# Optimization experiments

Measured on AMD Instinct MI355X. Metric: run time of the kernel, lower is better.

## Reference

```python
import jax, jax.numpy as jnp
import numpy as np

B, C = 4096, 50257

def setup_inputs() -> dict:
    key = jax.random.key(0)
    k1, k2 = jax.random.split(key)
    pred = jax.random.normal(k1, (B, C), dtype=jnp.float32)
    target = jax.random.randint(k2, (B,), 0, C, dtype=jnp.int64)
    return {"pred": pred, "target": target}

def reference(pred, target):
    # log_softmax over classes, gather the target log-prob per sample,
    # then -1/B * sum (the original's per-class dict grouping sums to the same total).
    logp = jax.nn.log_softmax(pred, axis=1)          # [B, C]
    gathered = jnp.take_along_axis(logp, target[:, None], axis=1)[:, 0]  # [B]
    Bf = pred.shape[0]
    return -jnp.sum(gathered) / Bf
```

## Files before the change

kernel.cpp:

```cpp
#include <hip/hip_runtime.h>

#define NROWS 4096
#define NCLASS 50257
#define BLK 256
#define U 8
#define DEFER_THR 8.0f

__global__ __launch_bounds__(BLK) void ce_row_kernel(
    const float* __restrict__ pred,
    const int* __restrict__ target,
    float* __restrict__ row_loss) {
    const int row = blockIdx.x;
    const float* __restrict__ p = pred + (size_t)row * NCLASS;
    const int tid = threadIdx.x;

    float m = -3.4e38f;
    float l = 0.0f;

    const int head = (int)(((16u - (unsigned)((size_t)p & 15u)) & 15u) >> 2);
    if (tid < head) {
        m = p[tid];
        l = 1.0f;
    }

    const float4* __restrict__ pv = (const float4*)(p + head);
    const int nvec = (NCLASS - head) >> 2;

    const int CHUNK = U * BLK;
    const int nchunk = nvec / CHUNK;

    for (int c = 0; c < nchunk; ++c) {
        const int base = c * CHUNK + tid;

        float4 v[U];
        #pragma unroll
        for (int k = 0; k < U; ++k) v[k] = pv[base + k * BLK];

        float cm = -3.4e38f;
        #pragma unroll
        for (int k = 0; k < U; ++k) {
            cm = fmaxf(cm,
                       fmaxf(fmaxf(v[k].x, v[k].y), fmaxf(v[k].z, v[k].w)));
        }

        if (cm > m + DEFER_THR) {
            l *= __expf(m - cm);
            m = cm;
        }

        float s = 0.0f;
        #pragma unroll
        for (int k = 0; k < U; ++k) {
            s += __expf(v[k].x - m) + __expf(v[k].y - m)
               + __expf(v[k].z - m) + __expf(v[k].w - m);
        }
        l += s;
    }

    for (int i = nchunk * CHUNK + tid; i < nvec; i += BLK) {
        float4 v = pv[i];
        float vm = fmaxf(fmaxf(v.x, v.y), fmaxf(v.z, v.w));
        if (vm > m + DEFER_THR) {
            l *= __expf(m - vm);
            m = vm;
        }
        l += __expf(v.x - m) + __expf(v.y - m)
           + __expf(v.z - m) + __expf(v.w - m);
    }
    for (int j = head + (nvec << 2) + tid; j < NCLASS; j += BLK) {
        float x = p[j];
        if (x > m + DEFER_THR) {
            l *= __expf(m - x);
            m = x;
        }
        l += __expf(x - m);
    }

    #pragma unroll
    for (int off = 32; off > 0; off >>= 1) {
        float om = __shfl_down(m, off, 64);
        float ol = __shfl_down(l, off, 64);
        float nm = fmaxf(m, om);
        l = l * __expf(m - nm) + ol * __expf(om - nm);
        m = nm;
    }

    __shared__ float sm[BLK / 64];
    __shared__ float sl[BLK / 64];
    const int wave = tid >> 6;
    const int lane = tid & 63;
    if (lane == 0) { sm[wave] = m; sl[wave] = l; }
    __syncthreads();

    if (tid == 0) {
        m = sm[0]; l = sl[0];
        #pragma unroll
        for (int w = 1; w < BLK / 64; ++w) {
            float om = sm[w], ol = sl[w];
            float nm = fmaxf(m, om);
            l = l * __expf(m - nm) + ol * __expf(om - nm);
            m = nm;
        }
        const int t = target[row];
        row_loss[row] = -(p[t] - m - __logf(l));
    }
}

__global__ __launch_bounds__(BLK) void ce_reduce_kernel(
    const float* __restrict__ row_loss,
    float* __restrict__ out) {
    const int tid = threadIdx.x;
    float s = 0.0f;
    for (int i = tid; i < NROWS; i += BLK) s += row_loss[i];

    #pragma unroll
    for (int off = 32; off > 0; off >>= 1) s += __shfl_down(s, off, 64);

    __shared__ float sw[BLK / 64];
    if ((tid & 63) == 0) sw[tid >> 6] = s;
    __syncthreads();

    if (tid == 0) {
        float t = 0.0f;
        #pragma unroll
        for (int w = 0; w < BLK / 64; ++w) t += sw[w];
        out[0] = t * (1.0f / (float)NROWS);
    }
}

extern "C" void kernel_launch(void* const* d_in, const int* in_sizes, int n_in,
                              void* d_out, int out_size, void* d_ws, size_t ws_size,
                              hipStream_t stream) {
    const float* pred = (const float*)d_in[0];
    const int* target = (const int*)d_in[1];
    float* out = (float*)d_out;
    float* row_loss = (float*)d_ws;

    ce_row_kernel<<<NROWS, BLK, 0, stream>>>(pred, target, row_loss);
    ce_reduce_kernel<<<1, BLK, 0, stream>>>(row_loss, out);
}
```

Baseline: 1.014 ms.

## Split each row across four blocks and merge partial softmax stats in finisher

Each row's class range is split into four parts, each handled by its own block that writes a partial max and sum-exp to workspace. A single-block finish kernel merges the four partials per row, gathers the target logit and reduces to the loss. The unroll factor drops to 4 and launch bounds request 6 blocks per CU. This raises block count and occupancy to better saturate HBM bandwidth on the 823 MB read, at the cost of extra workspace traffic, unaligned head handling per part, and a heavier serial finisher that does 4096 scattered target gathers in one block.

```diff
diff --git a/kernel.cpp b/kernel.cpp
--- a/kernel.cpp
+++ b/kernel.cpp
@@ -3,15 +3,21 @@
 #define NROWS 4096
 #define NCLASS 50257
 #define BLK 256
-#define U 8
+#define NSPLIT 4
+#define QLEN ((NCLASS + NSPLIT - 1) / NSPLIT)
+#define U 4
 #define DEFER_THR 8.0f
 
-__global__ __launch_bounds__(BLK) void ce_row_kernel(
+__global__ __launch_bounds__(BLK, 6) void ce_part_kernel(
     const float* __restrict__ pred,
-    const int* __restrict__ target,
-    float* __restrict__ row_loss) {
-    const int row = blockIdx.x;
-    const float* __restrict__ p = pred + (size_t)row * NCLASS;
+    float* __restrict__ mbuf,
+    float* __restrict__ lbuf) {
+    const int bid = blockIdx.x;
+    const int row  = bid >> 2;
+    const int part = bid & 3;
+    const int begin = part * QLEN;
+    const int n = ((begin + QLEN) < NCLASS ? QLEN : (NCLASS - begin));
+    const float* __restrict__ p = pred + (size_t)row * NCLASS + begin;
     const int tid = threadIdx.x;
 
     float m = -3.4e38f;
@@ -24,7 +30,7 @@
     }
 
     const float4* __restrict__ pv = (const float4*)(p + head);
-    const int nvec = (NCLASS - head) >> 2;
+    const int nvec = (n - head) >> 2;
 
     const int CHUNK = U * BLK;
     const int nchunk = nvec / CHUNK;
@@ -67,7 +73,7 @@
         l += __expf(v.x - m) + __expf(v.y - m)
            + __expf(v.z - m) + __expf(v.w - m);
     }
-    for (int j = head + (nvec << 2) + tid; j < NCLASS; j += BLK) {
+    for (int j = head + (nvec << 2) + tid; j < n; j += BLK) {
         float x = p[j];
         if (x > m + DEFER_THR) {
             l *= __expf(m - x);
@@ -101,17 +107,33 @@
             l = l * __expf(m - nm) + ol * __expf(om - nm);
             m = nm;
         }
-        const int t = target[row];
-        row_loss[row] = -(p[t] - m - __logf(l));
+        mbuf[part * NROWS + row] = m;
+        lbuf[part * NROWS + row] = l;
     }
 }
 
-__global__ __launch_bounds__(BLK) void ce_reduce_kernel(
-    const float* __restrict__ row_loss,
+__global__ __launch_bounds__(BLK) void ce_finish_kernel(
+    const float* __restrict__ pred,
+    const int* __restrict__ target,
+    const float* __restrict__ mbuf,
+    const float* __restrict__ lbuf,
     float* __restrict__ out) {
     const int tid = threadIdx.x;
     float s = 0.0f;
-    for (int i = tid; i < NROWS; i += BLK) s += row_loss[i];
+    for (int row = tid; row < NROWS; row += BLK) {
+        float m = mbuf[row];
+        float l = lbuf[row];
+        #pragma unroll
+        for (int q = 1; q < NSPLIT; ++q) {
+            float om = mbuf[q * NROWS + row];
+            float ol = lbuf[q * NROWS + row];
+            float nm = fmaxf(m, om);
+            l = l * __expf(m - nm) + ol * __expf(om - nm);
+            m = nm;
+        }
+        const int t = target[row];
+        s += -(pred[(size_t)row * NCLASS + t] - m - __logf(l));
+    }
 
     #pragma unroll
     for (int off = 32; off > 0; off >>= 1) s += __shfl_down(s, off, 64);
@@ -134,8 +156,9 @@
     const float* pred = (const float*)d_in[0];
     const int* target = (const int*)d_in[1];
     float* out = (float*)d_out;
-    float* row_loss = (float*)d_ws;
+    float* mbuf = (float*)d_ws;
+    float* lbuf = (float*)d_ws + NSPLIT * NROWS;
 
-    ce_row_kernel<<<NROWS, BLK, 0, stream>>>(pred, target, row_loss);
-    ce_reduce_kernel<<<1, BLK, 0, stream>>>(row_loss, out);
+    ce_part_kernel<<<NROWS * NSPLIT, BLK, 0, stream>>>(pred, mbuf, lbuf);
+    ce_finish_kernel<<<1, BLK, 0, stream>>>(pred, target, mbuf, lbuf, out);
 }
```

Result: no change. 1.023 ms (+0.9%).
